# Performance work log

Hardware: AMD Instinct MI355X
Metric: run time of the kernel (lower is better)

## Reference

```python
import jax, jax.numpy as jnp
import numpy as np

FRAME_PERIOD = 80   # samples per frame
IR_LENGTH = 2000    # filter length L (taps = L-1)
N_FFT = 4096


def setup_inputs() -> dict:
    key = jax.random.key(0)
    k1, k2 = jax.random.split(key)
    x = jax.random.normal(k1, (2, 24000), dtype=jnp.float32)          # waveform, T = 300*80
    mc = jax.random.normal(k2, (2, 300, 25), dtype=jnp.float32) * 0.1  # mel-cepstrum (B, N, M+1)
    return {"x": x, "mc": mc}


def _c2min_phase_ir(c):
    # cepstrum -> minimum-phase impulse response: ifft(exp(fft(c))) truncated.
    # (alpha=0, gamma=0 makes mgc2ir exactly this FFT-based conversion.)
    C = jnp.fft.fft(c, n=N_FFT, axis=-1)
    h = jnp.fft.ifft(jnp.exp(C), axis=-1).real[..., :IR_LENGTH]
    return h


def _linear_interpolate(h):
    # (B, N, L) frame-rate filters -> (B, N*P, L) sample-rate filters,
    # linear interpolation between consecutive frames, last frame replicated.
    B, N, L = h.shape
    P = FRAME_PERIOD
    h_next = jnp.concatenate([h[:, 1:], h[:, -1:]], axis=1)
    w = (jnp.arange(P, dtype=h.dtype) / P)[None, None, :, None]  # (1,1,P,1)
    y = h[:, :, None, :] * (1.0 - w) + h_next[:, :, None, :] * w  # (B,N,P,L)
    return y.reshape(B, N * P, L)


def reference(x, mc):
    L = IR_LENGTH
    h = _c2min_phase_ir(mc)      # (B, N, L) minimum-phase IR
    h = jnp.flip(h, axis=-1)     # phase == 'minimum': flip taps
    h = _linear_interpolate(h)   # (B, T, L)
    T = h.shape[1]
    # causal padding (taps, 0) then unfold into overlapping windows
    x_pad = jnp.pad(x, ((0, 0), (L - 1, 0)))
    idx = jnp.arange(T)[:, None] + jnp.arange(L)[None, :]  # (T, L)
    windows = x_pad[:, idx]                                # (B, T, L)
    y = jnp.sum(windows * h, axis=-1)                      # (B, T)
    return y
```

## Files before the change

### kernel.cpp

```cpp
#include <hip/hip_runtime.h>
#include <math.h>

#define IR_LEN  2000
#define PFRAME  80
#define NFRAMES 300
#define NBATCH  2
#define NROWS   (NBATCH*NFRAMES)
#define T_TOTAL (NFRAMES*PFRAME)
#define NCOEF   25
#define TWO_PI  6.283185307179586f
#define GS      68
#define XWN     2160
#define XWPAD   2432

#define XPHYS(B) ((B) + (((B) >> 5) << 2))

__device__ __forceinline__ void fsincos(float a, float* s, float* c) {
    *s = __sinf(a); *c = __cosf(a);
}

__global__ __launch_bounds__(256) void minphase_fir_fused(
        const float* __restrict__ mc, const float* __restrict__ x,
        float* __restrict__ y) {
    __shared__ __align__(16) float U[8704];
    __shared__ __align__(16) float xws[XWPAD];
    __shared__ float csh[NCOEF];
    float* const EHr = U;
    float* const EHi = U + 4096;
    float* const Gr  = U;
    float* const Gi  = U + 4352;
    float* const hU  = U;
    float* const red = U + 4224;

    const int row   = blockIdx.x;
    const int batch = row / NFRAMES;
    const int frame = row - batch * NFRAMES;
    const int t0    = frame * PFRAME;
    const int t     = threadIdx.x;

    if (t < NCOEF) csh[t] = mc[row * NCOEF + t];

    {
        const float* xb = x + batch * T_TOTAL;
        for (int j = t; j < XWN; j += 256) {
            const int xi = t0 - 2079 + j;
            const float v = (xi >= 0 && xi < T_TOTAL) ? xb[xi] : 0.0f;
            xws[XPHYS(j)] = v;
        }
    }
    __syncthreads();

    {
        float bs, bc; fsincos(-(TWO_PI / 4096.0f) * (float)t, &bs, &bc);
        const float SC =  0.923879532511287f;
        const float SS = -0.382683432365090f;
        #pragma unroll 4
        for (int ii = 0; ii < 8; ii++) {
            const int f = t + 256 * ii;
            const float wc = bc, ws = bs;
            { const float nr = bc * SC - bs * SS;
              const float ni = bc * SS + bs * SC;
              bc = nr; bs = ni; }
            float cr = 1.0f, ci = 0.0f, Cr = 0.0f, Ci = 0.0f;
            #pragma unroll
            for (int k = 0; k < NCOEF; k++) {
                const float cc = csh[k];
                Cr += cc * cr; Ci += cc * ci;
                const float nr = cr * wc - ci * ws;
                const float ni = cr * ws + ci * wc;
                cr = nr; ci = ni;
            }
            const float m = __expf(Cr);
            float si, co; fsincos(Ci, &si, &co);
            const float er = m * co, ei = m * si;
            EHr[f] = er; EHi[f] = ei;
            if (f > 0) { EHr[4096 - f] = er; EHi[4096 - f] = -ei; }
        }
        if (t == 0) {
            float Cr = 0.0f, Ci = 0.0f;
            float cr = 1.0f, ci = 0.0f;
            #pragma unroll
            for (int k = 0; k < NCOEF; k++) {
                Cr += csh[k] * cr; Ci += csh[k] * ci;
                cr = -cr; ci = -ci;
            }
            const float m = __expf(Cr);
            float si, co; fsincos(Ci, &si, &co);
            EHr[2048] = m * co; EHi[2048] = m * si;
        }
    }
    __syncthreads();

    {
        const int b0 = (t & 15) * 4;
        const int d0 = (t >> 4) * 2;
        float Ter[2][4], Tei[2][4], Tor[2][4], Toi[2][4];
        #pragma unroll
        for (int j = 0; j < 2; j++)
            #pragma unroll
            for (int i = 0; i < 4; i++) {
                Ter[j][i] = 0.0f; Tei[j][i] = 0.0f;
                Tor[j][i] = 0.0f; Toi[j][i] = 0.0f;
            }
        float rr[2], ri[2], wr[2], wi[2];
        #pragma unroll
        for (int j = 0; j < 2; j++) {
            float s, c; fsincos((TWO_PI / 32.0f) * (float)(d0 + j), &s, &c);
            wr[j] = c; wi[j] = s; rr[j] = 1.0f; ri[j] = 0.0f;
        }
        float4 vre = *(const float4*)&EHr[b0];
        float4 vie = *(const float4*)&EHi[b0];
        float4 vro = *(const float4*)&EHr[64 + b0];
        float4 vio = *(const float4*)&EHi[64 + b0];
        #pragma unroll 4
        for (int a2 = 0; a2 < 32; a2++) {
            const float4 cre = vre, cie = vie, cro = vro, cio = vio;
            if (a2 < 31) {
                const int nb = 128 * (a2 + 1) + b0;
                vre = *(const float4*)&EHr[nb];
                vie = *(const float4*)&EHi[nb];
                vro = *(const float4*)&EHr[nb + 64];
                vio = *(const float4*)&EHi[nb + 64];
            }
            const float ere[4] = {cre.x, cre.y, cre.z, cre.w};
            const float eie[4] = {cie.x, cie.y, cie.z, cie.w};
            const float ero[4] = {cro.x, cro.y, cro.z, cro.w};
            const float eio[4] = {cio.x, cio.y, cio.z, cio.w};
            #pragma unroll
            for (int j = 0; j < 2; j++) {
                #pragma unroll
                for (int i = 0; i < 4; i++) {
                    Ter[j][i] += ere[i] * rr[j] - eie[i] * ri[j];
                    Tei[j][i] += ere[i] * ri[j] + eie[i] * rr[j];
                    Tor[j][i] += ero[i] * rr[j] - eio[i] * ri[j];
                    Toi[j][i] += ero[i] * ri[j] + eio[i] * rr[j];
                }
                const float nr = rr[j] * wr[j] - ri[j] * wi[j];
                const float ni = rr[j] * wi[j] + ri[j] * wr[j];
                rr[j] = nr; ri[j] = ni;
            }
        }
        __syncthreads();

        float os[2], oc[2];
        #pragma unroll
        for (int j = 0; j < 2; j++)
            fsincos((TWO_PI / 64.0f) * (float)(d0 + j), &os[j], &oc[j]);
        #pragma unroll
        for (int i = 0; i < 4; i++) {
            const int b = b0 + i;
            float gpr[2], gpi[2], gmr[2], gmi[2];
            #pragma unroll
            for (int j = 0; j < 2; j++) {
                const int d = d0 + j;
                const float ur = oc[j] * Tor[j][i] - os[j] * Toi[j][i];
                const float ui = oc[j] * Toi[j][i] + os[j] * Tor[j][i];
                const float pr = Ter[j][i] + ur, pi = Tei[j][i] + ui;
                const float mr = Ter[j][i] - ur, mi = Tei[j][i] - ui;
                float s, c;
                fsincos((TWO_PI / 4096.0f) * (float)(b * d), &s, &c);
                gpr[j] = pr * c - pi * s; gpi[j] = pr * s + pi * c;
                fsincos((TWO_PI / 4096.0f) * (float)(b * (d + 32)), &s, &c);
                gmr[j] = mr * c - mi * s; gmi[j] = mr * s + mi * c;
            }
            *(float2*)&Gr[b * GS + d0]      = make_float2(gpr[0], gpr[1]);
            *(float2*)&Gi[b * GS + d0]      = make_float2(gpi[0], gpi[1]);
            *(float2*)&Gr[b * GS + d0 + 32] = make_float2(gmr[0], gmr[1]);
            *(float2*)&Gi[b * GS + d0 + 32] = make_float2(gmi[0], gmi[1]);
        }
    }
    __syncthreads();

    float hv[4][2];
    int   dl_, cg_;
    {
        const int dl = (t & 31) * 2;
        const int cg = t >> 5;
        dl_ = dl; cg_ = cg;
        float swi_, swr_; fsincos((TWO_PI / 64.0f) * (float)cg, &swi_, &swr_);
        const float swr = swr_, swi = swi_;
        float rr = 1.0f, ri = 0.0f;
        float acc00 = 0, acc01 = 0, acc10 = 0, acc11 = 0;
        float acc20 = 0, acc21 = 0, acc30 = 0, acc31 = 0;
        int bb = 0;

#define S2C 0.70710678118654752f
#define STEP2(f8r, f8i, f16r, f16i, f24r, f24i)                                \
        {                                                                      \
            const float2 g_r = *(const float2*)&Gr[bb * GS + dl];              \
            const float2 g_i = *(const float2*)&Gi[bb * GS + dl];              \
            acc00 += g_r.x * rr - g_i.x * ri;                                  \
            acc01 += g_r.y * rr - g_i.y * ri;                                  \
            { const float tr = rr*(f8r) - ri*(f8i), ti = rr*(f8i) + ri*(f8r);  \
              acc10 += g_r.x * tr - g_i.x * ti;                                \
              acc11 += g_r.y * tr - g_i.y * ti; }                              \
            { const float tr = rr*(f16r) - ri*(f16i), ti = rr*(f16i) + ri*(f16r); \
              acc20 += g_r.x * tr - g_i.x * ti;                                \
              acc21 += g_r.y * tr - g_i.y * ti; }                              \
            { const float tr = rr*(f24r) - ri*(f24i), ti = rr*(f24i) + ri*(f24r); \
              acc30 += g_r.x * tr - g_i.x * ti;                                \
              acc31 += g_r.y * tr - g_i.y * ti; }                              \
            { const float nr = rr * swr - ri * swi;                            \
              const float ni = rr * swi + ri * swr;                            \
              rr = nr; ri = ni; }                                              \
            bb++;                                                              \
        }

        for (int grp = 0; grp < 8; grp++) {
            STEP2( 1.0f, 0.0f,   1.0f, 0.0f,   1.0f, 0.0f)
            STEP2( S2C,  S2C,    0.0f, 1.0f,  -S2C,  S2C)
            STEP2( 0.0f, 1.0f,  -1.0f, 0.0f,   0.0f,-1.0f)
            STEP2(-S2C,  S2C,    0.0f,-1.0f,   S2C,  S2C)
            STEP2(-1.0f, 0.0f,   1.0f, 0.0f,  -1.0f, 0.0f)
            STEP2(-S2C, -S2C,    0.0f, 1.0f,   S2C, -S2C)
            STEP2( 0.0f,-1.0f,  -1.0f, 0.0f,   0.0f, 1.0f)
            STEP2( S2C, -S2C,    0.0f,-1.0f,  -S2C, -S2C)
        }
#undef STEP2
        const float sc = 1.0f / 4096.0f;
        hv[0][0] = acc00 * sc; hv[0][1] = acc01 * sc;
        hv[1][0] = acc10 * sc; hv[1][1] = acc11 * sc;
        hv[2][0] = acc20 * sc; hv[2][1] = acc21 * sc;
        hv[3][0] = acc30 * sc; hv[3][1] = acc31 * sc;
    }
    __syncthreads();

    #pragma unroll
    for (int v = 0; v < 4; v++) {
        const int c = cg_ + 8 * v;
        const int n = 64 * c + dl_;
        if (n < IR_LEN)     hU[n]     = hv[v][0];
        if (n + 1 < IR_LEN) hU[n + 1] = hv[v][1];
    }
    __syncthreads();

    if (t < 240) {
        const int o0 = (t % 20) * 8;
        const int kc = t / 20;
        const int kb = kc * 168;
        const int ns = (kc == 11) ? 38 : 42;
        float s0[8] = {0,0,0,0,0,0,0,0};
        int Bo = o0 + 1996 - kb;
        float4 w1 = *(const float4*)&xws[XPHYS(Bo + 4)];
        float4 w2 = *(const float4*)&xws[XPHYS(Bo + 8)];
        for (int s = 0; s < ns; s++) {
            const float4 w0 = *(const float4*)&xws[XPHYS(Bo)];
            const float4 ha = *(const float4*)&hU[kb + 4 * s];
            const float wv[12] = {w0.x, w0.y, w0.z, w0.w,
                                  w1.x, w1.y, w1.z, w1.w,
                                  w2.x, w2.y, w2.z, w2.w};
            const float hav[4] = {ha.x, ha.y, ha.z, ha.w};
            #pragma unroll
            for (int jo = 0; jo < 8; jo++) {
                #pragma unroll
                for (int jk = 0; jk < 4; jk++) {
                    s0[jo] += hav[jk] * wv[3 + jo - jk];
                }
            }
            w2 = w1; w1 = w0; Bo -= 4;
        }
        const int rb = kc * 168 + o0;
        *(float4*)&red[rb]     = make_float4(s0[0], s0[1], s0[2], s0[3]);
        *(float4*)&red[rb + 4] = make_float4(s0[4], s0[5], s0[6], s0[7]);
    }
    __syncthreads();

    if (t < 160) {
        float z = 0.0f;
        #pragma unroll
        for (int kc = 0; kc < 12; kc++) z += red[kc * 168 + t];
        const int o = t;
        const int tout = t0 - PFRAME + o;
        float wgt = (o < PFRAME) ? (float)o * (1.0f / PFRAME)
                                 : (float)(160 - o) * (1.0f / PFRAME);
        if (frame == NFRAMES - 1 && o >= PFRAME) wgt = 1.0f;
        if (tout >= 0) {
            atomicAdd(&y[batch * T_TOTAL + tout], wgt * z);
        }
    }
}

extern "C" void kernel_launch(void* const* d_in, const int* in_sizes, int n_in,
                              void* d_out, int out_size, void* d_ws, size_t ws_size,
                              hipStream_t stream) {
    const float* x  = (const float*)d_in[0];
    const float* mc = (const float*)d_in[1];
    float* y = (float*)d_out;

    hipMemsetAsync(y, 0, (size_t)out_size * sizeof(float), stream);
    minphase_fir_fused<<<NROWS, 256, 0, stream>>>(mc, x, y);
}
```

Measured before the change: 95.43 us.

## Exploit Hermitian symmetry in inverse FFT to halve twiddle-stage work

The inverse FFT is restructured around the conjugate symmetry of the real-output spectrum. Only 128 threads now compute the first-stage columns for bins 0..31, and 64 threads compute the self-conjugate bin 32 separately. The final stage accumulates only bins 1..31 and reconstructs the real output as G0 plus a signed G32 term plus twice the accumulated sum. This roughly halves the work and the shared-memory footprint of the G buffer, at the cost of divergent thread roles and extra special-case code paths.

```diff
diff --git a/kernel.cpp b/kernel.cpp
--- a/kernel.cpp
+++ b/kernel.cpp
@@ -28,7 +28,7 @@
     float* const EHr = U;
     float* const EHi = U + 4096;
     float* const Gr  = U;
-    float* const Gi  = U + 4352;
+    float* const Gi  = U + 2244;
     float* const hU  = U;
     float* const red = U + 4224;
 
@@ -92,81 +92,114 @@
     __syncthreads();
 
     {
-        const int b0 = (t & 15) * 4;
-        const int d0 = (t >> 4) * 2;
         float Ter[2][4], Tei[2][4], Tor[2][4], Toi[2][4];
-        #pragma unroll
-        for (int j = 0; j < 2; j++)
-            #pragma unroll
-            for (int i = 0; i < 4; i++) {
-                Ter[j][i] = 0.0f; Tei[j][i] = 0.0f;
-                Tor[j][i] = 0.0f; Toi[j][i] = 0.0f;
-            }
-        float rr[2], ri[2], wr[2], wi[2];
-        #pragma unroll
-        for (int j = 0; j < 2; j++) {
-            float s, c; fsincos((TWO_PI / 32.0f) * (float)(d0 + j), &s, &c);
-            wr[j] = c; wi[j] = s; rr[j] = 1.0f; ri[j] = 0.0f;
-        }
-        float4 vre = *(const float4*)&EHr[b0];
-        float4 vie = *(const float4*)&EHi[b0];
-        float4 vro = *(const float4*)&EHr[64 + b0];
-        float4 vio = *(const float4*)&EHi[64 + b0];
-        #pragma unroll 4
-        for (int a2 = 0; a2 < 32; a2++) {
-            const float4 cre = vre, cie = vie, cro = vro, cio = vio;
-            if (a2 < 31) {
-                const int nb = 128 * (a2 + 1) + b0;
-                vre = *(const float4*)&EHr[nb];
-                vie = *(const float4*)&EHi[nb];
-                vro = *(const float4*)&EHr[nb + 64];
-                vio = *(const float4*)&EHi[nb + 64];
-            }
-            const float ere[4] = {cre.x, cre.y, cre.z, cre.w};
-            const float eie[4] = {cie.x, cie.y, cie.z, cie.w};
-            const float ero[4] = {cro.x, cro.y, cro.z, cro.w};
-            const float eio[4] = {cio.x, cio.y, cio.z, cio.w};
-            #pragma unroll
-            for (int j = 0; j < 2; j++) {
+        float cTer = 0.0f, cTei = 0.0f, cTor = 0.0f, cToi = 0.0f;
+
+        if (t < 128) {
+            const int b0 = (t & 7) * 4;
+            const int d0 = ((t >> 3) & 15) * 2;
+            #pragma unroll
+            for (int j = 0; j < 2; j++)
                 #pragma unroll
                 for (int i = 0; i < 4; i++) {
-                    Ter[j][i] += ere[i] * rr[j] - eie[i] * ri[j];
-                    Tei[j][i] += ere[i] * ri[j] + eie[i] * rr[j];
-                    Tor[j][i] += ero[i] * rr[j] - eio[i] * ri[j];
-                    Toi[j][i] += ero[i] * ri[j] + eio[i] * rr[j];
-                }
-                const float nr = rr[j] * wr[j] - ri[j] * wi[j];
-                const float ni = rr[j] * wi[j] + ri[j] * wr[j];
-                rr[j] = nr; ri[j] = ni;
+                    Ter[j][i] = 0.0f; Tei[j][i] = 0.0f;
+                    Tor[j][i] = 0.0f; Toi[j][i] = 0.0f;
+                }
+            float rr[2], ri[2], wr[2], wi[2];
+            #pragma unroll
+            for (int j = 0; j < 2; j++) {
+                float s, c; fsincos((TWO_PI / 32.0f) * (float)(d0 + j), &s, &c);
+                wr[j] = c; wi[j] = s; rr[j] = 1.0f; ri[j] = 0.0f;
+            }
+            float4 vre = *(const float4*)&EHr[b0];
+            float4 vie = *(const float4*)&EHi[b0];
+            float4 vro = *(const float4*)&EHr[64 + b0];
+            float4 vio = *(const float4*)&EHi[64 + b0];
+            #pragma unroll 4
+            for (int a2 = 0; a2 < 32; a2++) {
+                const float4 cre = vre, cie = vie, cro = vro, cio = vio;
+                if (a2 < 31) {
+                    const int nb = 128 * (a2 + 1) + b0;
+                    vre = *(const float4*)&EHr[nb];
+                    vie = *(const float4*)&EHi[nb];
+                    vro = *(const float4*)&EHr[nb + 64];
+                    vio = *(const float4*)&EHi[nb + 64];
+                }
+                const float ere[4] = {cre.x, cre.y, cre.z, cre.w};
+                const float eie[4] = {cie.x, cie.y, cie.z, cie.w};
+                const float ero[4] = {cro.x, cro.y, cro.z, cro.w};
+                const float eio[4] = {cio.x, cio.y, cio.z, cio.w};
+                #pragma unroll
+                for (int j = 0; j < 2; j++) {
+                    #pragma unroll
+                    for (int i = 0; i < 4; i++) {
+                        Ter[j][i] += ere[i] * rr[j] - eie[i] * ri[j];
+                        Tei[j][i] += ere[i] * ri[j] + eie[i] * rr[j];
+                        Tor[j][i] += ero[i] * rr[j] - eio[i] * ri[j];
+                        Toi[j][i] += ero[i] * ri[j] + eio[i] * rr[j];
+                    }
+                    const float nr = rr[j] * wr[j] - ri[j] * wi[j];
+                    const float ni = rr[j] * wi[j] + ri[j] * wr[j];
+                    rr[j] = nr; ri[j] = ni;
+                }
+            }
+        } else if (t < 192) {
+            const int d = t - 128;
+            float sw, cw; fsincos((TWO_PI / 32.0f) * (float)d, &sw, &cw);
+            float rr = 1.0f, ri = 0.0f;
+            #pragma unroll 4
+            for (int a2 = 0; a2 < 32; a2++) {
+                const float ee_r = EHr[128 * a2 + 32];
+                const float ee_i = EHi[128 * a2 + 32];
+                const float eo_r = EHr[128 * a2 + 96];
+                const float eo_i = EHi[128 * a2 + 96];
+                cTer += ee_r * rr - ee_i * ri;
+                cTei += ee_r * ri + ee_i * rr;
+                cTor += eo_r * rr - eo_i * ri;
+                cToi += eo_r * ri + eo_i * rr;
+                const float nr = rr * cw - ri * sw;
+                const float ni = rr * sw + ri * cw;
+                rr = nr; ri = ni;
             }
         }
         __syncthreads();
 
-        float os[2], oc[2];
-        #pragma unroll
-        for (int j = 0; j < 2; j++)
-            fsincos((TWO_PI / 64.0f) * (float)(d0 + j), &os[j], &oc[j]);
-        #pragma unroll
-        for (int i = 0; i < 4; i++) {
-            const int b = b0 + i;
-            float gpr[2], gpi[2], gmr[2], gmi[2];
-            #pragma unroll
-            for (int j = 0; j < 2; j++) {
-                const int d = d0 + j;
-                const float ur = oc[j] * Tor[j][i] - os[j] * Toi[j][i];
-                const float ui = oc[j] * Toi[j][i] + os[j] * Tor[j][i];
-                const float pr = Ter[j][i] + ur, pi = Tei[j][i] + ui;
-                const float mr = Ter[j][i] - ur, mi = Tei[j][i] - ui;
-                float s, c;
-                fsincos((TWO_PI / 4096.0f) * (float)(b * d), &s, &c);
-                gpr[j] = pr * c - pi * s; gpi[j] = pr * s + pi * c;
-                fsincos((TWO_PI / 4096.0f) * (float)(b * (d + 32)), &s, &c);
-                gmr[j] = mr * c - mi * s; gmi[j] = mr * s + mi * c;
-            }
-            *(float2*)&Gr[b * GS + d0]      = make_float2(gpr[0], gpr[1]);
-            *(float2*)&Gi[b * GS + d0]      = make_float2(gpi[0], gpi[1]);
-            *(float2*)&Gr[b * GS + d0 + 32] = make_float2(gmr[0], gmr[1]);
-            *(float2*)&Gi[b * GS + d0 + 32] = make_float2(gmi[0], gmi[1]);
+        if (t < 128) {
+            const int b0 = (t & 7) * 4;
+            const int d0 = ((t >> 3) & 15) * 2;
+            float os[2], oc[2];
+            #pragma unroll
+            for (int j = 0; j < 2; j++)
+                fsincos((TWO_PI / 64.0f) * (float)(d0 + j), &os[j], &oc[j]);
+            #pragma unroll
+            for (int i = 0; i < 4; i++) {
+                const int b = b0 + i;
+                float gpr[2], gpi[2], gmr[2], gmi[2];
+                #pragma unroll
+                for (int j = 0; j < 2; j++) {
+                    const int d = d0 + j;
+                    const float ur = oc[j] * Tor[j][i] - os[j] * Toi[j][i];
+                    const float ui = oc[j] * Toi[j][i] + os[j] * Tor[j][i];
+                    const float pr = Ter[j][i] + ur, pi = Tei[j][i] + ui;
+                    const float mr = Ter[j][i] - ur, mi = Tei[j][i] - ui;
+                    float s, c;
+                    fsincos((TWO_PI / 4096.0f) * (float)(b * d), &s, &c);
+                    gpr[j] = pr * c - pi * s; gpi[j] = pr * s + pi * c;
+                    fsincos((TWO_PI / 4096.0f) * (float)(b * (d + 32)), &s, &c);
+                    gmr[j] = mr * c - mi * s; gmi[j] = mr * s + mi * c;
+                }
+                *(float2*)&Gr[b * GS + d0]      = make_float2(gpr[0], gpr[1]);
+                *(float2*)&Gi[b * GS + d0]      = make_float2(gpi[0], gpi[1]);
+                *(float2*)&Gr[b * GS + d0 + 32] = make_float2(gmr[0], gmr[1]);
+                *(float2*)&Gi[b * GS + d0 + 32] = make_float2(gmi[0], gmi[1]);
+            }
+        } else if (t < 192) {
+            const int d = t - 128;
+            float s64, c64; fsincos((TWO_PI / 64.0f) * (float)d, &s64, &c64);
+            const float Gre = cTer + (c64 * cTor - s64 * cToi);
+            const float Gim = cTei + (c64 * cToi + s64 * cTor);
+            float s128, c128; fsincos((TWO_PI / 128.0f) * (float)d, &s128, &c128);
+            Gr[32 * GS + d] = Gre * c128 - Gim * s128;
         }
     }
     __syncthreads();
@@ -179,10 +212,10 @@
         dl_ = dl; cg_ = cg;
         float swi_, swr_; fsincos((TWO_PI / 64.0f) * (float)cg, &swi_, &swr_);
         const float swr = swr_, swi = swi_;
-        float rr = 1.0f, ri = 0.0f;
+        float rr = swr, ri = swi;
         float acc00 = 0, acc01 = 0, acc10 = 0, acc11 = 0;
         float acc20 = 0, acc21 = 0, acc30 = 0, acc31 = 0;
-        int bb = 0;
+        int bb = 1;
 
 #define S2C 0.70710678118654752f
 #define STEP2(f8r, f8i, f16r, f16i, f24r, f24i)                                \
@@ -206,7 +239,14 @@
             bb++;                                                              \
         }
 
-        for (int grp = 0; grp < 8; grp++) {
+        STEP2( S2C,  S2C,    0.0f, 1.0f,  -S2C,  S2C)
+        STEP2( 0.0f, 1.0f,  -1.0f, 0.0f,   0.0f,-1.0f)
+        STEP2(-S2C,  S2C,    0.0f,-1.0f,   S2C,  S2C)
+        STEP2(-1.0f, 0.0f,   1.0f, 0.0f,  -1.0f, 0.0f)
+        STEP2(-S2C, -S2C,    0.0f, 1.0f,   S2C, -S2C)
+        STEP2( 0.0f,-1.0f,  -1.0f, 0.0f,   0.0f, 1.0f)
+        STEP2( S2C, -S2C,    0.0f,-1.0f,  -S2C, -S2C)
+        for (int grp = 0; grp < 3; grp++) {
             STEP2( 1.0f, 0.0f,   1.0f, 0.0f,   1.0f, 0.0f)
             STEP2( S2C,  S2C,    0.0f, 1.0f,  -S2C,  S2C)
             STEP2( 0.0f, 1.0f,  -1.0f, 0.0f,   0.0f,-1.0f)
@@ -217,11 +257,19 @@
             STEP2( S2C, -S2C,    0.0f,-1.0f,  -S2C, -S2C)
         }
 #undef STEP2
+
+        const float g0a  = Gr[dl],           g0b  = Gr[dl + 1];
+        const float g32a = Gr[32 * GS + dl], g32b = Gr[32 * GS + dl + 1];
+        const float sgn  = (cg & 1) ? -1.0f : 1.0f;
         const float sc = 1.0f / 4096.0f;
-        hv[0][0] = acc00 * sc; hv[0][1] = acc01 * sc;
-        hv[1][0] = acc10 * sc; hv[1][1] = acc11 * sc;
-        hv[2][0] = acc20 * sc; hv[2][1] = acc21 * sc;
-        hv[3][0] = acc30 * sc; hv[3][1] = acc31 * sc;
+        hv[0][0] = (g0a + sgn * g32a + 2.0f * acc00) * sc;
+        hv[0][1] = (g0b + sgn * g32b + 2.0f * acc01) * sc;
+        hv[1][0] = (g0a + sgn * g32a + 2.0f * acc10) * sc;
+        hv[1][1] = (g0b + sgn * g32b + 2.0f * acc11) * sc;
+        hv[2][0] = (g0a + sgn * g32a + 2.0f * acc20) * sc;
+        hv[2][1] = (g0b + sgn * g32b + 2.0f * acc21) * sc;
+        hv[3][0] = (g0a + sgn * g32a + 2.0f * acc30) * sc;
+        hv[3][1] = (g0b + sgn * g32b + 2.0f * acc31) * sc;
     }
     __syncthreads();
 
```

After: 110.3 us. 15.6% more time.

## Exploit Hermitian symmetry to halve inverse-FFT work in minimum-phase IR

Applied to the files above, without the earlier changes.

Stores only half of the exp(C) spectrum and reads the mirrored half through conjugate indexing, so the mirror writes are dropped. The stage-2 transform now computes only 32 of the 64 b-columns. The real-output last stage uses symmetry: it accumulates bins 1..31 doubled and adds the DC and Nyquist columns separately, with the Nyquist column computed by a new small reduction into Pr/Pq. This roughly halves the arithmetic of the spectral stages, at the cost of extra shared memory, an extra reduction pass, and more intricate index logic with some strided scalar LDS reads.

```diff
diff --git a/kernel.cpp b/kernel.cpp
--- a/kernel.cpp
+++ b/kernel.cpp
@@ -9,7 +9,7 @@
 #define T_TOTAL (NFRAMES*PFRAME)
 #define NCOEF   25
 #define TWO_PI  6.283185307179586f
-#define GS      68
+#define GS2     66
 #define XWN     2160
 #define XWPAD   2432
 
@@ -22,13 +22,15 @@
 __global__ __launch_bounds__(256) void minphase_fir_fused(
         const float* __restrict__ mc, const float* __restrict__ x,
         float* __restrict__ y) {
-    __shared__ __align__(16) float U[8704];
+    __shared__ __align__(16) float U[8972];
     __shared__ __align__(16) float xws[XWPAD];
     __shared__ float csh[NCOEF];
     float* const EHr = U;
-    float* const EHi = U + 4096;
-    float* const Gr  = U;
-    float* const Gi  = U + 4352;
+    float* const EHi = U + 2052;
+    float* const Gr  = U + 4104;
+    float* const Gi  = U + 6282;
+    float* const Pr  = U + 8460;
+    float* const Pq  = U + 8716;
     float* const hU  = U;
     float* const red = U + 4224;
 
@@ -72,9 +74,7 @@
             }
             const float m = __expf(Cr);
             float si, co; fsincos(Ci, &si, &co);
-            const float er = m * co, ei = m * si;
-            EHr[f] = er; EHi[f] = ei;
-            if (f > 0) { EHr[4096 - f] = er; EHi[4096 - f] = -ei; }
+            EHr[f] = m * co; EHi[f] = m * si;
         }
         if (t == 0) {
             float Cr = 0.0f, Ci = 0.0f;
@@ -92,44 +92,30 @@
     __syncthreads();
 
     {
-        const int b0 = (t & 15) * 4;
-        const int d0 = (t >> 4) * 2;
-        float Ter[2][4], Tei[2][4], Tor[2][4], Toi[2][4];
-        #pragma unroll
-        for (int j = 0; j < 2; j++)
-            #pragma unroll
-            for (int i = 0; i < 4; i++) {
-                Ter[j][i] = 0.0f; Tei[j][i] = 0.0f;
-                Tor[j][i] = 0.0f; Toi[j][i] = 0.0f;
-            }
+        const int bq = t & 15, dq = t >> 4;
+        const int b0 = 2 * bq;
+        const int d0 = 2 * dq;
+        float Ter[2][2] = {{0,0},{0,0}}, Tei[2][2] = {{0,0},{0,0}};
+        float Tor[2][2] = {{0,0},{0,0}}, Toi[2][2] = {{0,0},{0,0}};
         float rr[2], ri[2], wr[2], wi[2];
         #pragma unroll
         for (int j = 0; j < 2; j++) {
             float s, c; fsincos((TWO_PI / 32.0f) * (float)(d0 + j), &s, &c);
             wr[j] = c; wi[j] = s; rr[j] = 1.0f; ri[j] = 0.0f;
         }
-        float4 vre = *(const float4*)&EHr[b0];
-        float4 vie = *(const float4*)&EHi[b0];
-        float4 vro = *(const float4*)&EHr[64 + b0];
-        float4 vio = *(const float4*)&EHi[64 + b0];
         #pragma unroll 4
-        for (int a2 = 0; a2 < 32; a2++) {
-            const float4 cre = vre, cie = vie, cro = vro, cio = vio;
-            if (a2 < 31) {
-                const int nb = 128 * (a2 + 1) + b0;
-                vre = *(const float4*)&EHr[nb];
-                vie = *(const float4*)&EHi[nb];
-                vro = *(const float4*)&EHr[nb + 64];
-                vio = *(const float4*)&EHi[nb + 64];
-            }
-            const float ere[4] = {cre.x, cre.y, cre.z, cre.w};
-            const float eie[4] = {cie.x, cie.y, cie.z, cie.w};
-            const float ero[4] = {cro.x, cro.y, cro.z, cro.w};
-            const float eio[4] = {cio.x, cio.y, cio.z, cio.w};
+        for (int a2 = 0; a2 < 16; a2++) {
+            const int base = 128 * a2 + b0;
+            const float2 re = *(const float2*)&EHr[base];
+            const float2 ie = *(const float2*)&EHi[base];
+            const float2 ro = *(const float2*)&EHr[base + 64];
+            const float2 io = *(const float2*)&EHi[base + 64];
+            const float ere[2] = {re.x, re.y}, eie[2] = {ie.x, ie.y};
+            const float ero[2] = {ro.x, ro.y}, eio[2] = {io.x, io.y};
             #pragma unroll
             for (int j = 0; j < 2; j++) {
                 #pragma unroll
-                for (int i = 0; i < 4; i++) {
+                for (int i = 0; i < 2; i++) {
                     Ter[j][i] += ere[i] * rr[j] - eie[i] * ri[j];
                     Tei[j][i] += ere[i] * ri[j] + eie[i] * rr[j];
                     Tor[j][i] += ero[i] * rr[j] - eio[i] * ri[j];
@@ -140,33 +126,85 @@
                 rr[j] = nr; ri[j] = ni;
             }
         }
-        __syncthreads();
-
-        float os[2], oc[2];
-        #pragma unroll
-        for (int j = 0; j < 2; j++)
-            fsincos((TWO_PI / 64.0f) * (float)(d0 + j), &os[j], &oc[j]);
-        #pragma unroll
-        for (int i = 0; i < 4; i++) {
-            const int b = b0 + i;
-            float gpr[2], gpi[2], gmr[2], gmi[2];
+        #pragma unroll 4
+        for (int a2 = 16; a2 < 32; a2++) {
+            const int fe = 4096 - 128 * a2 - b0;
+            const int fo = fe - 64;
+            const float ere[2] = {EHr[fe], EHr[fe - 1]};
+            const float eme[2] = {EHi[fe], EHi[fe - 1]};
+            const float ero[2] = {EHr[fo], EHr[fo - 1]};
+            const float emo[2] = {EHi[fo], EHi[fo - 1]};
             #pragma unroll
             for (int j = 0; j < 2; j++) {
-                const int d = d0 + j;
-                const float ur = oc[j] * Tor[j][i] - os[j] * Toi[j][i];
-                const float ui = oc[j] * Toi[j][i] + os[j] * Tor[j][i];
-                const float pr = Ter[j][i] + ur, pi = Tei[j][i] + ui;
-                const float mr = Ter[j][i] - ur, mi = Tei[j][i] - ui;
-                float s, c;
-                fsincos((TWO_PI / 4096.0f) * (float)(b * d), &s, &c);
-                gpr[j] = pr * c - pi * s; gpi[j] = pr * s + pi * c;
-                fsincos((TWO_PI / 4096.0f) * (float)(b * (d + 32)), &s, &c);
-                gmr[j] = mr * c - mi * s; gmi[j] = mr * s + mi * c;
-            }
-            *(float2*)&Gr[b * GS + d0]      = make_float2(gpr[0], gpr[1]);
-            *(float2*)&Gi[b * GS + d0]      = make_float2(gpi[0], gpi[1]);
-            *(float2*)&Gr[b * GS + d0 + 32] = make_float2(gmr[0], gmr[1]);
-            *(float2*)&Gi[b * GS + d0 + 32] = make_float2(gmi[0], gmi[1]);
+                #pragma unroll
+                for (int i = 0; i < 2; i++) {
+                    Ter[j][i] += ere[i] * rr[j] + eme[i] * ri[j];
+                    Tei[j][i] += ere[i] * ri[j] - eme[i] * rr[j];
+                    Tor[j][i] += ero[i] * rr[j] + emo[i] * ri[j];
+                    Toi[j][i] += ero[i] * ri[j] - emo[i] * rr[j];
+                }
+                const float nr = rr[j] * wr[j] - ri[j] * wi[j];
+                const float ni = rr[j] * wi[j] + ri[j] * wr[j];
+                rr[j] = nr; ri[j] = ni;
+            }
+        }
+        {
+            float os[2], oc[2];
+            #pragma unroll
+            for (int j = 0; j < 2; j++)
+                fsincos((TWO_PI / 64.0f) * (float)(d0 + j), &os[j], &oc[j]);
+            #pragma unroll
+            for (int i = 0; i < 2; i++) {
+                const int b = b0 + i;
+                float gpr[2], gpi[2], gmr[2], gmi[2];
+                #pragma unroll
+                for (int j = 0; j < 2; j++) {
+                    const int d = d0 + j;
+                    const float ur = oc[j] * Tor[j][i] - os[j] * Toi[j][i];
+                    const float ui = oc[j] * Toi[j][i] + os[j] * Tor[j][i];
+                    const float pr = Ter[j][i] + ur, pi = Tei[j][i] + ui;
+                    const float mr = Ter[j][i] - ur, mi = Tei[j][i] - ui;
+                    float s, c;
+                    fsincos((TWO_PI / 4096.0f) * (float)(b * d), &s, &c);
+                    gpr[j] = pr * c - pi * s; gpi[j] = pr * s + pi * c;
+                    fsincos((TWO_PI / 4096.0f) * (float)(b * (d + 32)), &s, &c);
+                    gmr[j] = mr * c - mi * s; gmi[j] = mr * s + mi * c;
+                }
+                *(float2*)&Gr[b * GS2 + d0]      = make_float2(gpr[0], gpr[1]);
+                *(float2*)&Gi[b * GS2 + d0]      = make_float2(gpi[0], gpi[1]);
+                *(float2*)&Gr[b * GS2 + d0 + 32] = make_float2(gmr[0], gmr[1]);
+                *(float2*)&Gi[b * GS2 + d0 + 32] = make_float2(gmi[0], gmi[1]);
+            }
+        }
+        {
+            const int pd = t & 63;
+            const int pq = t >> 6;
+            const int m4 = (pq * pd) & 3;
+            float prr, pri;
+            if      (m4 == 0) { prr = 1.0f;  pri = 0.0f;  }
+            else if (m4 == 1) { prr = 0.0f;  pri = 1.0f;  }
+            else if (m4 == 2) { prr = -1.0f; pri = 0.0f;  }
+            else              { prr = 0.0f;  pri = -1.0f; }
+            float pws, pwc; fsincos((TWO_PI / 64.0f) * (float)pd, &pws, &pwc);
+            float Ar = 0.0f, Ai = 0.0f;
+            #pragma unroll 4
+            for (int s = 0; s < 16; s++) {
+                const int a = 16 * pq + s;
+                float er, ei;
+                if (pq < 2) {
+                    const int idx = 64 * a + 32;
+                    er = EHr[idx]; ei = EHi[idx];
+                } else {
+                    const int fi = 4064 - 64 * a;
+                    er = EHr[fi]; ei = -EHi[fi];
+                }
+                Ar += er * prr - ei * pri;
+                Ai += er * pri + ei * prr;
+                const float nr = prr * pwc - pri * pws;
+                const float ni = prr * pws + pri * pwc;
+                prr = nr; pri = ni;
+            }
+            Pr[t] = Ar; Pq[t] = Ai;
         }
     }
     __syncthreads();
@@ -179,16 +217,16 @@
         dl_ = dl; cg_ = cg;
         float swi_, swr_; fsincos((TWO_PI / 64.0f) * (float)cg, &swi_, &swr_);
         const float swr = swr_, swi = swi_;
-        float rr = 1.0f, ri = 0.0f;
+        float rr = swr, ri = swi;
         float acc00 = 0, acc01 = 0, acc10 = 0, acc11 = 0;
         float acc20 = 0, acc21 = 0, acc30 = 0, acc31 = 0;
-        int bb = 0;
+        int bb = 1;
 
 #define S2C 0.70710678118654752f
 #define STEP2(f8r, f8i, f16r, f16i, f24r, f24i)                                \
         {                                                                      \
-            const float2 g_r = *(const float2*)&Gr[bb * GS + dl];              \
-            const float2 g_i = *(const float2*)&Gi[bb * GS + dl];              \
+            const float2 g_r = *(const float2*)&Gr[bb * GS2 + dl];             \
+            const float2 g_i = *(const float2*)&Gi[bb * GS2 + dl];             \
             acc00 += g_r.x * rr - g_i.x * ri;                                  \
             acc01 += g_r.y * rr - g_i.y * ri;                                  \
             { const float tr = rr*(f8r) - ri*(f8i), ti = rr*(f8i) + ri*(f8r);  \
@@ -206,7 +244,14 @@
             bb++;                                                              \
         }
 
-        for (int grp = 0; grp < 8; grp++) {
+        STEP2( S2C,  S2C,    0.0f, 1.0f,  -S2C,  S2C)
+        STEP2( 0.0f, 1.0f,  -1.0f, 0.0f,   0.0f,-1.0f)
+        STEP2(-S2C,  S2C,    0.0f,-1.0f,   S2C,  S2C)
+        STEP2(-1.0f, 0.0f,   1.0f, 0.0f,  -1.0f, 0.0f)
+        STEP2(-S2C, -S2C,    0.0f, 1.0f,   S2C, -S2C)
+        STEP2( 0.0f,-1.0f,  -1.0f, 0.0f,   0.0f, 1.0f)
+        STEP2( S2C, -S2C,    0.0f,-1.0f,  -S2C, -S2C)
+        for (int grp = 0; grp < 3; grp++) {
             STEP2( 1.0f, 0.0f,   1.0f, 0.0f,   1.0f, 0.0f)
             STEP2( S2C,  S2C,    0.0f, 1.0f,  -S2C,  S2C)
             STEP2( 0.0f, 1.0f,  -1.0f, 0.0f,   0.0f,-1.0f)
@@ -217,11 +262,27 @@
             STEP2( S2C, -S2C,    0.0f,-1.0f,  -S2C, -S2C)
         }
 #undef STEP2
+
+        const float g0a = Gr[dl], g0b = Gr[dl + 1];
+        float g32[2];
+        #pragma unroll
+        for (int e = 0; e < 2; e++) {
+            const int d = dl + e;
+            const float sr = Pr[d] + Pr[64 + d] + Pr[128 + d] + Pr[192 + d];
+            const float si = Pq[d] + Pq[64 + d] + Pq[128 + d] + Pq[192 + d];
+            float ss, cc; fsincos((TWO_PI / 128.0f) * (float)d, &ss, &cc);
+            g32[e] = sr * cc - si * ss;
+        }
+        const float sgn = (cg & 1) ? -1.0f : 1.0f;
         const float sc = 1.0f / 4096.0f;
-        hv[0][0] = acc00 * sc; hv[0][1] = acc01 * sc;
-        hv[1][0] = acc10 * sc; hv[1][1] = acc11 * sc;
-        hv[2][0] = acc20 * sc; hv[2][1] = acc21 * sc;
-        hv[3][0] = acc30 * sc; hv[3][1] = acc31 * sc;
+        hv[0][0] = (g0a + sgn * g32[0] + 2.0f * acc00) * sc;
+        hv[0][1] = (g0b + sgn * g32[1] + 2.0f * acc01) * sc;
+        hv[1][0] = (g0a + sgn * g32[0] + 2.0f * acc10) * sc;
+        hv[1][1] = (g0b + sgn * g32[1] + 2.0f * acc11) * sc;
+        hv[2][0] = (g0a + sgn * g32[0] + 2.0f * acc20) * sc;
+        hv[2][1] = (g0b + sgn * g32[1] + 2.0f * acc21) * sc;
+        hv[3][0] = (g0a + sgn * g32[0] + 2.0f * acc30) * sc;
+        hv[3][1] = (g0b + sgn * g32[1] + 2.0f * acc31) * sc;
     }
     __syncthreads();
 
```

Measured after the change: 108.9 us. 14.1% more time.
